# Kernel tuning notes

Hardware: AMD Instinct MI355X
Metric: run time of the kernel (lower is better)

## Reference

```python
import jax, jax.numpy as jnp
import numpy as np

B, N, F, G, M, E = 8, 512, 64, 64, 4, 4
L0 = 256          # NodeEmbedding hidden width (layers[0])
ALPHA = 0.5
EPS = 1e-5        # BatchNorm eps (training mode, batch stats)
NEG = -9e15       # masked-out logit value from the torch code


def _glorot(key, shape):
    # matches repo's glorot(): U(-s, s), s = sqrt(6/(fan_in+fan_out)) on last two dims
    s = float(np.sqrt(6.0 / (shape[-2] + shape[-1])))
    return jax.random.uniform(key, shape, minval=-s, maxval=s, dtype=jnp.float32)


def _xavier(key, shape, gain=1.0):
    s = gain * float(np.sqrt(6.0 / (shape[-2] + shape[-1])))
    return jax.random.uniform(key, shape, minval=-s, maxval=s, dtype=jnp.float32)


def setup_inputs() -> dict:
    key = jax.random.key(0)
    ks = jax.random.split(key, 8)
    A = jax.random.randint(ks[0], (B, E, N, N), 0, 2).astype(jnp.int32)  # dense 0/1 adjacency per edge cat
    X = jax.random.normal(ks[1], (B, N, F), dtype=jnp.float32)
    Ws = _glorot(ks[2], (E, M * F, G))                     # per-edge-cat stacked multi-head proj
    a1 = _xavier(ks[3], (E, M * G, 1), gain=1.414)
    a2 = _xavier(ks[4], (E, M * G, 1), gain=1.414)
    W_emb1 = _xavier(ks[5], (F, M * E * G))                # Embedding1: Linear(M*E*G -> F, no bias)
    W2a = _xavier(ks[6], (L0, F))                          # NodeEmbedding linear0: F -> L0
    W2b = _xavier(ks[7], (F, L0))                          # NodeEmbedding linear1: L0 -> F
    return {"A": A, "X": X, "Ws": Ws, "a1": a1, "a2": a2,
            "W_emb1": W_emb1, "W2a": W2a, "W2b": W2b, "mini_batch": 1}


def _bn(x):
    # BatchNorm1d in training mode, weight=1, bias=0, biased variance
    mu = x.mean(axis=0)
    var = x.var(axis=0)
    return (x - mu) / jnp.sqrt(var + EPS)


def reference(A, X, Ws, a1, a2, W_emb1, W2a, W2b, mini_batch):
    Wsr = Ws.reshape(E, M, F, G)        # per edge-cat, per head projection
    a1r = a1.reshape(E, M, G)
    a2r = a2.reshape(E, M, G)

    # Wh[b,e,m,n,g] = X[b] @ Ws[e] head m
    Wh = jnp.einsum('bnf,emfg->bemng', X, Wsr)
    s1 = jnp.einsum('bemng,emg->bemn', Wh, a1r)
    s2 = jnp.einsum('bemng,emg->bemn', Wh, a2r)
    logits = jax.nn.leaky_relu(s1[..., :, None] + s2[..., None, :])  # [B,E,M,N,N]
    logits = jnp.where(A[:, :, None, :, :] > 0, logits, NEG)
    att = jax.nn.softmax(logits, axis=-1)                            # softmax over neighbors (dim=1 of NxN)
    H = jax.nn.elu(jnp.einsum('bemij,bemjg->bemig', att, Wh))        # [B,E,M,N,G]

    # layout matches torch reshapes: feature index = m*(E*G) + e*G + g
    H = H.transpose(0, 3, 2, 1, 4).reshape(B * N, M * E * G)
    H = H @ W_emb1.T                                                 # Embedding1
    Xf = X.reshape(B * N, F)
    H = _bn((1.0 - ALPHA) * H + ALPHA * Xf)                          # BN1 with residual mix

    # NodeEmbedding: Linear -> BN -> ELU -> Linear
    Z = jax.nn.elu(_bn(H @ W2a.T)) @ W2b.T
    Z = _bn(H + Z)                                                   # BN2 residual
    return Z.reshape(B, N, F)
```

## Files before the change

### kernel.cpp

```cpp
#include <hip/hip_runtime.h>
#include <math.h>

#define B_   8
#define N_   512
#define F_   64
#define G_   64
#define M_   4
#define E_   4
#define MEG  1024

typedef __attribute__((ext_vector_type(8))) __bf16 bf16x8;
typedef __attribute__((ext_vector_type(4))) float f32x4;
typedef unsigned short ush;

static __device__ __forceinline__ ush bfu(float x) { __bf16 h = (__bf16)x; return __builtin_bit_cast(ush, h); }
static __device__ __forceinline__ bf16x8 asbf(int4 v) { return __builtin_bit_cast(bf16x8, v); }
static __device__ __forceinline__ bf16x8 cvt8(float4 a, float4 b) {
  bf16x8 r;
  r[0] = (__bf16)a.x; r[1] = (__bf16)a.y; r[2] = (__bf16)a.z; r[3] = (__bf16)a.w;
  r[4] = (__bf16)b.x; r[5] = (__bf16)b.y; r[6] = (__bf16)b.z; r[7] = (__bf16)b.w;
  return r;
}

__global__ void __launch_bounds__(256) k1_wh(const float* __restrict__ X, const float* __restrict__ Ws,
                                             const float* __restrict__ a1, const float* __restrict__ a2,
                                             const int* __restrict__ A,
                                             ush* __restrict__ WhF, float* __restrict__ s1,
                                             float2* __restrict__ E2, unsigned* __restrict__ Amask) {
  const int tid = threadIdx.x, lane = tid & 63, w = tid >> 6, c = lane & 15, grp = lane >> 4;
  const int blk = blockIdx.x, nt = blk & 7, em = (blk >> 3) & 15, b = blk >> 7;
  const int n0 = nt * 64, bem = b * 16 + em;

  __shared__ __align__(16) ush xl[2][4][64][8];
  __shared__ __align__(16) ush wl[2][4][64][8];
  __shared__ float c1b[64], c2b[64];
  __shared__ __align__(16) ush st[4096];

  {
    const int w2 = blk * 256 + tid;
    const int* ap = A + (w2 >> 4) * 512 + (w2 & 15) * 32;
    unsigned bits = 0;
#pragma unroll
    for (int kq = 0; kq < 32; kq += 4) {
      int4 v = *(const int4*)(ap + kq);
      bits |= (v.x > 0 ? 1u : 0u) << kq;
      bits |= (v.y > 0 ? 1u : 0u) << (kq + 1);
      bits |= (v.z > 0 ? 1u : 0u) << (kq + 2);
      bits |= (v.w > 0 ? 1u : 0u) << (kq + 3);
    }
    Amask[w2] = bits;
  }

  {
    const int row = tid >> 2, cg = tid & 3;
    const int t = row >> 4, cc = row & 15;
    const float* xp = X + (b * 512 + n0 + row) * 64 + cg * 16;
#pragma unroll
    for (int q4 = 0; q4 < 4; ++q4) {
      float4 v = ((const float4*)xp)[q4];
      float vals[4] = {v.x, v.y, v.z, v.w};
#pragma unroll
      for (int u = 0; u < 4; ++u) {
        const int f = cg * 16 + q4 * 4 + u;
        xl[f >> 5][t][((f >> 3) & 3) * 16 + cc][f & 7] = bfu(vals[u]);
      }
    }
  }
  {
    const int f = tid >> 2, gq = tid & 3;
    const int kk = f >> 5, gg = (f >> 3) & 3, ii = f & 7;
    const float* wp = Ws + em * 4096 + f * 64 + gq * 16;
    const float* p1 = a1 + em * 64 + gq * 16;
    const float* p2 = a2 + em * 64 + gq * 16;
    float d1 = 0.f, d2 = 0.f;
#pragma unroll
    for (int q4 = 0; q4 < 4; ++q4) {
      float4 v  = ((const float4*)wp)[q4];
      float4 va = ((const float4*)p1)[q4];
      float4 vb = ((const float4*)p2)[q4];
      float vals[4] = {v.x, v.y, v.z, v.w};
      float aa[4] = {va.x, va.y, va.z, va.w};
      float bb[4] = {vb.x, vb.y, vb.z, vb.w};
#pragma unroll
      for (int u = 0; u < 4; ++u) {
        const int g = gq * 16 + q4 * 4 + u;
        wl[kk][g >> 4][gg * 16 + (g & 15)][ii] = bfu(vals[u]);
        d1 = fmaf(vals[u], aa[u], d1);
        d2 = fmaf(vals[u], bb[u], d2);
      }
    }
    d1 += __shfl_xor(d1, 1); d1 += __shfl_xor(d1, 2);
    d2 += __shfl_xor(d2, 1); d2 += __shfl_xor(d2, 2);
    if (gq == 0) { c1b[f] = d1; c2b[f] = d2; }
  }
  __syncthreads();

  f32x4 acc[4] = {};
#pragma unroll
  for (int kk = 0; kk < 2; ++kk) {
    bf16x8 af = asbf(*(const int4*)&wl[kk][w][lane][0]);
#pragma unroll
    for (int t = 0; t < 4; ++t) {
      bf16x8 bv = asbf(*(const int4*)&xl[kk][t][lane][0]);
      acc[t] = __builtin_amdgcn_mfma_f32_16x16x32_bf16(af, bv, acc[t], 0, 0, 0);
    }
  }
#pragma unroll
  for (int t = 0; t < 4; ++t) {
    const int sl = t >> 1;
    const int gp = (t & 1) * 2 + (c >> 3);
    const int ii = c & 7;
#pragma unroll
    for (int r = 0; r < 4; ++r)
      st[sl * 2048 + w * 512 + (gp * 16 + grp * 4 + r) * 8 + ii] = bfu(acc[t][r]);
  }
  if (w == 0) {
    f32x4 sacc[4] = {};
#pragma unroll
    for (int kk = 0; kk < 2; ++kk) {
      bf16x8 af;
#pragma unroll
      for (int i = 0; i < 8; ++i) {
        const int f = kk * 32 + grp * 8 + i;
        float v = (c == 0) ? c1b[f] : (c == 1) ? c2b[f] : 0.f;
        af[i] = (__bf16)v;
      }
#pragma unroll
      for (int t = 0; t < 4; ++t) {
        bf16x8 bv = asbf(*(const int4*)&xl[kk][t][lane][0]);
        sacc[t] = __builtin_amdgcn_mfma_f32_16x16x32_bf16(af, bv, sacc[t], 0, 0, 0);
      }
    }
    if (grp == 0) {
#pragma unroll
      for (int t = 0; t < 4; ++t) {
        float s2v = sacc[t][1];
        s1[bem * 512 + n0 + t * 16 + c] = sacc[t][0];
        E2[bem * 512 + n0 + t * 16 + c] = make_float2(__expf(s2v), __expf(0.01f * s2v));
      }
    }
  }
  __syncthreads();
  {
    int4* dst = (int4*)(WhF + bem * 32768 + nt * 4096);
    const int4* src = (const int4*)st;
    dst[tid * 2]     = src[tid * 2];
    dst[tid * 2 + 1] = src[tid * 2 + 1];
  }
}

__global__ void __launch_bounds__(256) k2_attn(const unsigned* __restrict__ Amask,
                                               const ush* __restrict__ WhF,
                                               const float* __restrict__ s1,
                                               const float2* __restrict__ E2,
                                               ush* __restrict__ Hb) {
  const int tid = threadIdx.x, lane = tid & 63, m = tid >> 6;
  const int grp = lane >> 4, col = lane & 15;
  const int blk = blockIdx.x;
  const int xcd = blk & 7, kk2 = blk >> 3;
  const int be = xcd * 4 + (kk2 >> 5), itile = kk2 & 31;
  const int b = be >> 2, e = be & 3;
  const int i0 = itile * 16;
  const int bem = be * 4 + m;

  __shared__ unsigned maskw[16][17];
  __shared__ float2 e2l[4][512];

  {
    const int row = tid >> 4, cc = tid & 15;
    maskw[row][cc] = Amask[(be * 512 + i0 + row) * 16 + cc];
  }
  {
    const float2* e2g = E2 + bem * 512;
#pragma unroll
    for (int t = 0; t < 8; ++t) e2l[m][t * 64 + lane] = e2g[t * 64 + lane];
  }
  __syncthreads();

  const float s1row = s1[bem * N_ + i0 + col];
  const float e1p = __expf(s1row);
  const float e1n = __expf(0.01f * s1row);
  const float te  = __expf(-s1row);

  const ush* whb = WhF + bem * 32768 + lane * 8;
  f32x4 acc0 = {0.f, 0.f, 0.f, 0.f};
  f32x4 acc1 = acc0, acc2 = acc0, acc3 = acc0, accs = acc0;
  bf16x8 ones;
#pragma unroll
  for (int i = 0; i < 8; ++i) ones[i] = (__bf16)1.0f;

  int4 c0 = *(const int4*)(whb + 0);
  int4 c1 = *(const int4*)(whb + 512);
  int4 c2 = *(const int4*)(whb + 1024);
  int4 c3 = *(const int4*)(whb + 1536);
#pragma unroll 4
  for (int s = 0; s < 16; ++s) {
    const int noff = ((s + 1) & 15) * 2048;
    int4 n0 = *(const int4*)(whb + noff);
    int4 n1 = *(const int4*)(whb + noff + 512);
    int4 n2 = *(const int4*)(whb + noff + 1024);
    int4 n3 = *(const int4*)(whb + noff + 1536);

    unsigned mb = maskw[col][s] >> (grp * 8);
    const float2* ep = &e2l[m][s * 32 + grp * 8];
    bf16x8 af;
#pragma unroll
    for (int i = 0; i < 8; ++i) {
      float2 q = ep[i];
      float p = (q.x > te) ? q.x * e1p : q.y * e1n;
      p = ((mb >> i) & 1u) ? p : 0.f;
      af[i] = (__bf16)p;
    }
    accs = __builtin_amdgcn_mfma_f32_16x16x32_bf16(af, ones, accs, 0, 0, 0);
    acc0 = __builtin_amdgcn_mfma_f32_16x16x32_bf16(af, asbf(c0), acc0, 0, 0, 0);
    acc1 = __builtin_amdgcn_mfma_f32_16x16x32_bf16(af, asbf(c1), acc1, 0, 0, 0);
    acc2 = __builtin_amdgcn_mfma_f32_16x16x32_bf16(af, asbf(c2), acc2, 0, 0, 0);
    acc3 = __builtin_amdgcn_mfma_f32_16x16x32_bf16(af, asbf(c3), acc3, 0, 0, 0);
    c0 = n0; c1 = n1; c2 = n2; c3 = n3;
  }

  ush* op = Hb + (b * N_ + i0 + grp * 4) * MEG + m * 256 + e * 64 + col;
#pragma unroll
  for (int r = 0; r < 4; ++r) {
    float sv2 = accs[r];
    float inv = sv2 > 0.f ? 1.f / sv2 : 0.f;
    float v0 = acc0[r] * inv; v0 = v0 > 0.f ? v0 : expm1f(v0);
    float v1 = acc1[r] * inv; v1 = v1 > 0.f ? v1 : expm1f(v1);
    float v2 = acc2[r] * inv; v2 = v2 > 0.f ? v2 : expm1f(v2);
    float v3 = acc3[r] * inv; v3 = v3 > 0.f ? v3 : expm1f(v3);
    op[r * MEG + 0]  = bfu(v0);
    op[r * MEG + 16] = bfu(v1);
    op[r * MEG + 32] = bfu(v2);
    op[r * MEG + 48] = bfu(v3);
  }
}

__global__ void __launch_bounds__(256) k3_emb(const ush* __restrict__ Hb, const float* __restrict__ W_emb1,
                                              const float* __restrict__ X, float* __restrict__ R,
                                              float* __restrict__ P2R) {
  const int tid = threadIdx.x, lane = tid & 63, w = tid >> 6, c = lane & 15, grp = lane >> 4;
  const int r0 = blockIdx.x * 16;
  const ush* ha = Hb + (r0 + c) * 1024 + grp * 8;
  const float* wbf = W_emb1 + (w * 16 + c) * 1024 + grp * 8;
  f32x4 accA = {}, accB = {};
#pragma unroll 8
  for (int kk = 0; kk < 32; kk += 2) {
    bf16x8 w0 = cvt8(*(const float4*)(wbf + kk * 32),      *(const float4*)(wbf + kk * 32 + 4));
    bf16x8 w1 = cvt8(*(const float4*)(wbf + kk * 32 + 32), *(const float4*)(wbf + kk * 32 + 36));
    accA = __builtin_amdgcn_mfma_f32_16x16x32_bf16(asbf(*(const int4*)(ha + kk * 32)), w0, accA, 0, 0, 0);
    accB = __builtin_amdgcn_mfma_f32_16x16x32_bf16(asbf(*(const int4*)(ha + kk * 32 + 32)), w1, accB, 0, 0, 0);
  }
  f32x4 acc = accA + accB;
  const int col = w * 16 + c;
  float s = 0.f, q = 0.f;
#pragma unroll
  for (int r = 0; r < 4; ++r) {
    int row = r0 + grp * 4 + r;
    float v = 0.5f * acc[r] + 0.5f * X[row * 64 + col];
    R[row * 64 + col] = v;
    s += v; q = fmaf(v, v, q);
  }
  s += __shfl_xor(s, 16); s += __shfl_xor(s, 32);
  q += __shfl_xor(q, 16); q += __shfl_xor(q, 32);
  if (grp == 0) { P2R[blockIdx.x * 128 + col] = s; P2R[blockIdx.x * 128 + 64 + col] = q; }
}

__global__ void __launch_bounds__(256) k4_node1(const float* __restrict__ R, const float* __restrict__ P2R,
                                                const float* __restrict__ W2a,
                                                float* __restrict__ T, float* __restrict__ P2T) {
  const int tid = threadIdx.x, lane = tid & 63, w = tid >> 6, c = lane & 15, grp = lane >> 4;
  const int r0 = blockIdx.x * 16, cb = w * 64;
  __shared__ float muR[64], rsR[64];
  if (tid < 128) {
    const int cc = tid & 63;
    float a = 0.f;
    for (int bk = 0; bk < 256; ++bk) a += P2R[bk * 128 + tid];
    if (tid < 64) muR[cc] = a * (1.f / 4096.f); else rsR[cc] = a;
  }
  __syncthreads();
  if (tid < 64) {
    float m = muR[tid];
    float v = rsR[tid] * (1.f / 4096.f) - m * m;
    rsR[tid] = rsqrtf(v + 1e-5f);
  }
  __syncthreads();

  f32x4 acc[4] = {};
#pragma unroll
  for (int kk = 0; kk < 2; ++kk) {
    const float* rp = R + (r0 + c) * 64 + kk * 32 + grp * 8;
    float4 v0 = *(const float4*)rp;
    float4 v1 = *(const float4*)(rp + 4);
    float vv[8] = {v0.x, v0.y, v0.z, v0.w, v1.x, v1.y, v1.z, v1.w};
    bf16x8 af;
#pragma unroll
    for (int i = 0; i < 8; ++i) {
      int f = kk * 32 + grp * 8 + i;
      af[i] = (__bf16)((vv[i] - muR[f]) * rsR[f]);
    }
#pragma unroll
    for (int ct = 0; ct < 4; ++ct) {
      const float* wp = W2a + (cb + ct * 16 + c) * 64 + kk * 32 + grp * 8;
      bf16x8 bv = cvt8(*(const float4*)wp, *(const float4*)(wp + 4));
      acc[ct] = __builtin_amdgcn_mfma_f32_16x16x32_bf16(af, bv, acc[ct], 0, 0, 0);
    }
  }
#pragma unroll
  for (int ct = 0; ct < 4; ++ct) {
    const int col = cb + ct * 16 + c;
    float s = 0.f, q = 0.f;
#pragma unroll
    for (int r = 0; r < 4; ++r) {
      float v = acc[ct][r];
      T[(r0 + grp * 4 + r) * 256 + col] = v;
      s += v; q = fmaf(v, v, q);
    }
    s += __shfl_xor(s, 16); s += __shfl_xor(s, 32);
    q += __shfl_xor(q, 16); q += __shfl_xor(q, 32);
    if (grp == 0) { P2T[blockIdx.x * 512 + col] = s; P2T[blockIdx.x * 512 + 256 + col] = q; }
  }
}

__global__ void __launch_bounds__(256) k5_node2(const float* __restrict__ T, const float* __restrict__ P2T,
                                                const float* __restrict__ W2b,
                                                const float* __restrict__ R, const float* __restrict__ P2R,
                                                float* __restrict__ S, float* __restrict__ P2S) {
  const int tid = threadIdx.x, lane = tid & 63, w = tid >> 6, c = lane & 15, grp = lane >> 4;
  const int r0 = blockIdx.x * 16;
  __shared__ float muT[256], rsT[256], muR[64], rsR[64];
  {
    float s = 0.f, q = 0.f;
    for (int bk = 0; bk < 256; ++bk) {
      s += P2T[bk * 512 + tid];
      q += P2T[bk * 512 + 256 + tid];
    }
    float m = s * (1.f / 4096.f);
    float v = q * (1.f / 4096.f) - m * m;
    muT[tid] = m; rsT[tid] = rsqrtf(v + 1e-5f);
  }
  if (tid < 128) {
    const int cc = tid & 63;
    float a = 0.f;
    for (int bk = 0; bk < 256; ++bk) a += P2R[bk * 128 + tid];
    if (tid < 64) muR[cc] = a * (1.f / 4096.f); else rsR[cc] = a;
  }
  __syncthreads();
  if (tid < 64) {
    float m = muR[tid];
    float v = rsR[tid] * (1.f / 4096.f) - m * m;
    rsR[tid] = rsqrtf(v + 1e-5f);
  }
  __syncthreads();

  f32x4 accA = {}, accB = {};
  const float* wrow = W2b + (w * 16 + c) * 256 + grp * 8;
  const float* trow = T + (r0 + c) * 256 + grp * 8;
#pragma unroll
  for (int kk = 0; kk < 8; ++kk) {
    float4 v0 = *(const float4*)(trow + kk * 32);
    float4 v1 = *(const float4*)(trow + kk * 32 + 4);
    float vv[8] = {v0.x, v0.y, v0.z, v0.w, v1.x, v1.y, v1.z, v1.w};
    bf16x8 af;
#pragma unroll
    for (int i = 0; i < 8; ++i) {
      int u = kk * 32 + grp * 8 + i;
      float t = (vv[i] - muT[u]) * rsT[u];
      t = t > 0.f ? t : expm1f(t);
      af[i] = (__bf16)t;
    }
    bf16x8 bv = cvt8(*(const float4*)(wrow + kk * 32), *(const float4*)(wrow + kk * 32 + 4));
    if (kk & 1) accB = __builtin_amdgcn_mfma_f32_16x16x32_bf16(af, bv, accB, 0, 0, 0);
    else        accA = __builtin_amdgcn_mfma_f32_16x16x32_bf16(af, bv, accA, 0, 0, 0);
  }
  f32x4 acc = accA + accB;
  const int col = w * 16 + c;
  const float mu = muR[col], rsv = rsR[col];
  float s = 0.f, q = 0.f;
#pragma unroll
  for (int r = 0; r < 4; ++r) {
    int row = r0 + grp * 4 + r;
    float v = acc[r] + (R[row * 64 + col] - mu) * rsv;
    S[row * 64 + col] = v;
    s += v; q = fmaf(v, v, q);
  }
  s += __shfl_xor(s, 16); s += __shfl_xor(s, 32);
  q += __shfl_xor(q, 16); q += __shfl_xor(q, 32);
  if (grp == 0) { P2S[blockIdx.x * 128 + col] = s; P2S[blockIdx.x * 128 + 64 + col] = q; }
}

__global__ void __launch_bounds__(256) k6_bn(const float* __restrict__ S, const float* __restrict__ P2S,
                                             float* __restrict__ out) {
  const int tid = threadIdx.x;
  const int r0 = blockIdx.x * 16;
  __shared__ float muS[64], rsS[64];
  if (tid < 128) {
    const int cc = tid & 63;
    float a = 0.f;
    for (int bk = 0; bk < 256; ++bk) a += P2S[bk * 128 + tid];
    if (tid < 64) muS[cc] = a * (1.f / 4096.f); else rsS[cc] = a;
  }
  __syncthreads();
  if (tid < 64) {
    float m = muS[tid];
    float v = rsS[tid] * (1.f / 4096.f) - m * m;
    rsS[tid] = rsqrtf(v + 1e-5f);
  }
  __syncthreads();
  const int f0 = (tid * 4) & 63;
  float4 v = *(const float4*)(S + r0 * 64 + tid * 4);
  float4 o;
  o.x = (v.x - muS[f0 + 0]) * rsS[f0 + 0];
  o.y = (v.y - muS[f0 + 1]) * rsS[f0 + 1];
  o.z = (v.z - muS[f0 + 2]) * rsS[f0 + 2];
  o.w = (v.w - muS[f0 + 3]) * rsS[f0 + 3];
  *(float4*)(out + r0 * 64 + tid * 4) = o;
}

extern "C" void kernel_launch(void* const* d_in, const int* in_sizes, int n_in,
                              void* d_out, int out_size, void* d_ws, size_t ws_size,
                              hipStream_t stream) {
  const int*   A      = (const int*)d_in[0];
  const float* X      = (const float*)d_in[1];
  const float* Ws     = (const float*)d_in[2];
  const float* a1     = (const float*)d_in[3];
  const float* a2     = (const float*)d_in[4];
  const float* W_emb1 = (const float*)d_in[5];
  const float* W2a    = (const float*)d_in[6];
  const float* W2b    = (const float*)d_in[7];
  float* out = (float*)d_out;

  float* ws = (float*)d_ws;
  ush*   Hb    = (ush*)d_ws;
  ush*   WhF   = (ush*)(ws + 2097152);
  float* s1    = ws + 4194304;
  float2* E2   = (float2*)(ws + 4259840);
  float* R     = ws + 4612096;
  float* T     = ws + 4874240;
  float* S     = ws + 5922816;
  float* P2R   = ws + 6184960;
  float* P2T   = ws + 6217728;
  float* P2S   = ws + 6348800;
  unsigned* Amask = (unsigned*)R;

  k1_wh<<<1024, 256, 0, stream>>>(X, Ws, a1, a2, A, WhF, s1, E2, Amask);
  k2_attn<<<1024, 256, 0, stream>>>(Amask, WhF, s1, E2, Hb);
  k3_emb<<<256, 256, 0, stream>>>(Hb, W_emb1, X, R, P2R);
  k4_node1<<<256, 256, 0, stream>>>(R, P2R, W2a, T, P2T);
  k5_node2<<<256, 256, 0, stream>>>(T, P2T, W2b, R, P2R, S, P2S);
  k6_bn<<<256, 256, 0, stream>>>(S, P2S, out);
}
```

Baseline: 96.71 us.

## Process two 16-row tiles per attention block to reuse Wh loads

Each k2_attn block now computes 32 query rows as two 16-row MFMA tiles that share the same Wh B-operand fragments. The prefetch distance grows to two steps and the grid is halved to 512 blocks. This halves the global Wh traffic per output row and amortises the mask and E2 staging. In exchange it needs twice the accumulator registers, may lower occupancy, and leaves fewer blocks to spread across CUs.

```diff
diff --git a/kernel.cpp b/kernel.cpp
--- a/kernel.cpp
+++ b/kernel.cpp
@@ -158,17 +158,18 @@
   const int grp = lane >> 4, col = lane & 15;
   const int blk = blockIdx.x;
   const int xcd = blk & 7, kk2 = blk >> 3;
-  const int be = xcd * 4 + (kk2 >> 5), itile = kk2 & 31;
+  const int be = xcd * 4 + (kk2 >> 4), itile = kk2 & 15;
   const int b = be >> 2, e = be & 3;
-  const int i0 = itile * 16;
+  const int i0 = itile * 32;
   const int bem = be * 4 + m;
 
-  __shared__ unsigned maskw[16][17];
+  __shared__ unsigned maskw[32][17];
   __shared__ float2 e2l[4][512];
 
   {
-    const int row = tid >> 4, cc = tid & 15;
-    maskw[row][cc] = Amask[(be * 512 + i0 + row) * 16 + cc];
+    const int i_0 = tid, i_1 = tid + 256;
+    maskw[i_0 >> 4][i_0 & 15] = Amask[(be * 512 + i0 + (i_0 >> 4)) * 16 + (i_0 & 15)];
+    maskw[i_1 >> 4][i_1 & 15] = Amask[(be * 512 + i0 + (i_1 >> 4)) * 16 + (i_1 & 15)];
   }
   {
     const float2* e2g = E2 + bem * 512;
@@ -177,61 +178,94 @@
   }
   __syncthreads();
 
-  const float s1row = s1[bem * N_ + i0 + col];
-  const float e1p = __expf(s1row);
-  const float e1n = __expf(0.01f * s1row);
-  const float te  = __expf(-s1row);
+  const float s1A = s1[bem * N_ + i0 + col];
+  const float s1B = s1[bem * N_ + i0 + 16 + col];
+  const float e1pA = __expf(s1A), e1nA = __expf(0.01f * s1A), teA = __expf(-s1A);
+  const float e1pB = __expf(s1B), e1nB = __expf(0.01f * s1B), teB = __expf(-s1B);
 
   const ush* whb = WhF + bem * 32768 + lane * 8;
-  f32x4 acc0 = {0.f, 0.f, 0.f, 0.f};
-  f32x4 acc1 = acc0, acc2 = acc0, acc3 = acc0, accs = acc0;
+  f32x4 a0A = {0.f, 0.f, 0.f, 0.f};
+  f32x4 a1A = a0A, a2A = a0A, a3A = a0A, sA = a0A;
+  f32x4 a0B = a0A, a1B = a0A, a2B = a0A, a3B = a0A, sB = a0A;
   bf16x8 ones;
 #pragma unroll
   for (int i = 0; i < 8; ++i) ones[i] = (__bf16)1.0f;
 
-  int4 c0 = *(const int4*)(whb + 0);
-  int4 c1 = *(const int4*)(whb + 512);
-  int4 c2 = *(const int4*)(whb + 1024);
-  int4 c3 = *(const int4*)(whb + 1536);
-#pragma unroll 4
+  int4 cA0 = *(const int4*)(whb + 0);
+  int4 cA1 = *(const int4*)(whb + 512);
+  int4 cA2 = *(const int4*)(whb + 1024);
+  int4 cA3 = *(const int4*)(whb + 1536);
+  int4 cB0 = *(const int4*)(whb + 2048);
+  int4 cB1 = *(const int4*)(whb + 2560);
+  int4 cB2 = *(const int4*)(whb + 3072);
+  int4 cB3 = *(const int4*)(whb + 3584);
+#pragma unroll
   for (int s = 0; s < 16; ++s) {
-    const int noff = ((s + 1) & 15) * 2048;
+    const int noff = ((s + 2) & 15) * 2048;
     int4 n0 = *(const int4*)(whb + noff);
     int4 n1 = *(const int4*)(whb + noff + 512);
     int4 n2 = *(const int4*)(whb + noff + 1024);
     int4 n3 = *(const int4*)(whb + noff + 1536);
 
-    unsigned mb = maskw[col][s] >> (grp * 8);
+    const unsigned mbA = maskw[col][s] >> (grp * 8);
+    const unsigned mbB = maskw[col + 16][s] >> (grp * 8);
     const float2* ep = &e2l[m][s * 32 + grp * 8];
-    bf16x8 af;
+    bf16x8 afA, afB;
 #pragma unroll
     for (int i = 0; i < 8; ++i) {
       float2 q = ep[i];
-      float p = (q.x > te) ? q.x * e1p : q.y * e1n;
-      p = ((mb >> i) & 1u) ? p : 0.f;
-      af[i] = (__bf16)p;
-    }
-    accs = __builtin_amdgcn_mfma_f32_16x16x32_bf16(af, ones, accs, 0, 0, 0);
-    acc0 = __builtin_amdgcn_mfma_f32_16x16x32_bf16(af, asbf(c0), acc0, 0, 0, 0);
-    acc1 = __builtin_amdgcn_mfma_f32_16x16x32_bf16(af, asbf(c1), acc1, 0, 0, 0);
-    acc2 = __builtin_amdgcn_mfma_f32_16x16x32_bf16(af, asbf(c2), acc2, 0, 0, 0);
-    acc3 = __builtin_amdgcn_mfma_f32_16x16x32_bf16(af, asbf(c3), acc3, 0, 0, 0);
-    c0 = n0; c1 = n1; c2 = n2; c3 = n3;
-  }
-
-  ush* op = Hb + (b * N_ + i0 + grp * 4) * MEG + m * 256 + e * 64 + col;
-#pragma unroll
-  for (int r = 0; r < 4; ++r) {
-    float sv2 = accs[r];
-    float inv = sv2 > 0.f ? 1.f / sv2 : 0.f;
-    float v0 = acc0[r] * inv; v0 = v0 > 0.f ? v0 : expm1f(v0);
-    float v1 = acc1[r] * inv; v1 = v1 > 0.f ? v1 : expm1f(v1);
-    float v2 = acc2[r] * inv; v2 = v2 > 0.f ? v2 : expm1f(v2);
-    float v3 = acc3[r] * inv; v3 = v3 > 0.f ? v3 : expm1f(v3);
-    op[r * MEG + 0]  = bfu(v0);
-    op[r * MEG + 16] = bfu(v1);
-    op[r * MEG + 32] = bfu(v2);
-    op[r * MEG + 48] = bfu(v3);
+      float pA = (q.x > teA) ? q.x * e1pA : q.y * e1nA;
+      pA = ((mbA >> i) & 1u) ? pA : 0.f;
+      afA[i] = (__bf16)pA;
+      float pB = (q.x > teB) ? q.x * e1pB : q.y * e1nB;
+      pB = ((mbB >> i) & 1u) ? pB : 0.f;
+      afB[i] = (__bf16)pB;
+    }
+    sA  = __builtin_amdgcn_mfma_f32_16x16x32_bf16(afA, ones, sA, 0, 0, 0);
+    sB  = __builtin_amdgcn_mfma_f32_16x16x32_bf16(afB, ones, sB, 0, 0, 0);
+    a0A = __builtin_amdgcn_mfma_f32_16x16x32_bf16(afA, asbf(cA0), a0A, 0, 0, 0);
+    a0B = __builtin_amdgcn_mfma_f32_16x16x32_bf16(afB, asbf(cA0), a0B, 0, 0, 0);
+    a1A = __builtin_amdgcn_mfma_f32_16x16x32_bf16(afA, asbf(cA1), a1A, 0, 0, 0);
+    a1B = __builtin_amdgcn_mfma_f32_16x16x32_bf16(afB, asbf(cA1), a1B, 0, 0, 0);
+    a2A = __builtin_amdgcn_mfma_f32_16x16x32_bf16(afA, asbf(cA2), a2A, 0, 0, 0);
+    a2B = __builtin_amdgcn_mfma_f32_16x16x32_bf16(afB, asbf(cA2), a2B, 0, 0, 0);
+    a3A = __builtin_amdgcn_mfma_f32_16x16x32_bf16(afA, asbf(cA3), a3A, 0, 0, 0);
+    a3B = __builtin_amdgcn_mfma_f32_16x16x32_bf16(afB, asbf(cA3), a3B, 0, 0, 0);
+    cA0 = cB0; cA1 = cB1; cA2 = cB2; cA3 = cB3;
+    cB0 = n0;  cB1 = n1;  cB2 = n2;  cB3 = n3;
+  }
+
+  {
+    ush* op = Hb + (b * N_ + i0 + grp * 4) * MEG + m * 256 + e * 64 + col;
+#pragma unroll
+    for (int r = 0; r < 4; ++r) {
+      float sv = sA[r];
+      float inv = sv > 0.f ? 1.f / sv : 0.f;
+      float v0 = a0A[r] * inv; v0 = v0 > 0.f ? v0 : expm1f(v0);
+      float v1 = a1A[r] * inv; v1 = v1 > 0.f ? v1 : expm1f(v1);
+      float v2 = a2A[r] * inv; v2 = v2 > 0.f ? v2 : expm1f(v2);
+      float v3 = a3A[r] * inv; v3 = v3 > 0.f ? v3 : expm1f(v3);
+      op[r * MEG + 0]  = bfu(v0);
+      op[r * MEG + 16] = bfu(v1);
+      op[r * MEG + 32] = bfu(v2);
+      op[r * MEG + 48] = bfu(v3);
+    }
+  }
+  {
+    ush* op = Hb + (b * N_ + i0 + 16 + grp * 4) * MEG + m * 256 + e * 64 + col;
+#pragma unroll
+    for (int r = 0; r < 4; ++r) {
+      float sv = sB[r];
+      float inv = sv > 0.f ? 1.f / sv : 0.f;
+      float v0 = a0B[r] * inv; v0 = v0 > 0.f ? v0 : expm1f(v0);
+      float v1 = a1B[r] * inv; v1 = v1 > 0.f ? v1 : expm1f(v1);
+      float v2 = a2B[r] * inv; v2 = v2 > 0.f ? v2 : expm1f(v2);
+      float v3 = a3B[r] * inv; v3 = v3 > 0.f ? v3 : expm1f(v3);
+      op[r * MEG + 0]  = bfu(v0);
+      op[r * MEG + 16] = bfu(v1);
+      op[r * MEG + 32] = bfu(v2);
+      op[r * MEG + 48] = bfu(v3);
+    }
   }
 }
 
@@ -443,7 +477,7 @@
   unsigned* Amask = (unsigned*)R;
 
   k1_wh<<<1024, 256, 0, stream>>>(X, Ws, a1, a2, A, WhF, s1, E2, Amask);
-  k2_attn<<<1024, 256, 0, stream>>>(Amask, WhF, s1, E2, Hb);
+  k2_attn<<<512, 256, 0, stream>>>(Amask, WhF, s1, E2, Hb);
   k3_emb<<<256, 256, 0, stream>>>(Hb, W_emb1, X, R, P2R);
   k4_node1<<<256, 256, 0, stream>>>(R, P2R, W2a, T, P2T);
   k5_node2<<<256, 256, 0, stream>>>(T, P2T, W2b, R, P2R, S, P2S);
```

Result: no change. 96.92 us (+0.2%).

## Widen tail kernels to 512 threads with split-K and parallel BN stat reductions

Applied to the files above, without the earlier changes.

Doubles the block size of the embedding and node-MLP kernels. The matmuls are split along K across two wave groups and the partial sums are combined through shared memory. The per-block reduction of batch-norm partial statistics is spread over all threads in chunks instead of a serial 256-iteration loop by a few threads. This targets latency in these small tail kernels, which run only 256 blocks, at the cost of extra syncthreads and shared memory.

```diff
diff --git a/kernel.cpp b/kernel.cpp
--- a/kernel.cpp
+++ b/kernel.cpp
@@ -235,57 +235,84 @@
   }
 }
 
-__global__ void __launch_bounds__(256) k3_emb(const ush* __restrict__ Hb, const float* __restrict__ W_emb1,
+__global__ void __launch_bounds__(512) k3_emb(const ush* __restrict__ Hb, const float* __restrict__ W_emb1,
                                               const float* __restrict__ X, float* __restrict__ R,
                                               float* __restrict__ P2R) {
-  const int tid = threadIdx.x, lane = tid & 63, w = tid >> 6, c = lane & 15, grp = lane >> 4;
+  const int tid = threadIdx.x, lane = tid & 63, w8 = tid >> 6, c = lane & 15, grp = lane >> 4;
+  const int wcol = w8 & 3, khalf = w8 >> 2;
   const int r0 = blockIdx.x * 16;
-  const ush* ha = Hb + (r0 + c) * 1024 + grp * 8;
-  const float* wbf = W_emb1 + (w * 16 + c) * 1024 + grp * 8;
+  __shared__ float part[4][64][4];
+
+  const ush* ha = Hb + (r0 + c) * 1024 + khalf * 512 + grp * 8;
+  const float* wbf = W_emb1 + (wcol * 16 + c) * 1024 + khalf * 512 + grp * 8;
   f32x4 accA = {}, accB = {};
 #pragma unroll 8
-  for (int kk = 0; kk < 32; kk += 2) {
+  for (int kk = 0; kk < 16; kk += 2) {
     bf16x8 w0 = cvt8(*(const float4*)(wbf + kk * 32),      *(const float4*)(wbf + kk * 32 + 4));
     bf16x8 w1 = cvt8(*(const float4*)(wbf + kk * 32 + 32), *(const float4*)(wbf + kk * 32 + 36));
     accA = __builtin_amdgcn_mfma_f32_16x16x32_bf16(asbf(*(const int4*)(ha + kk * 32)), w0, accA, 0, 0, 0);
     accB = __builtin_amdgcn_mfma_f32_16x16x32_bf16(asbf(*(const int4*)(ha + kk * 32 + 32)), w1, accB, 0, 0, 0);
   }
   f32x4 acc = accA + accB;
-  const int col = w * 16 + c;
-  float s = 0.f, q = 0.f;
-#pragma unroll
-  for (int r = 0; r < 4; ++r) {
-    int row = r0 + grp * 4 + r;
-    float v = 0.5f * acc[r] + 0.5f * X[row * 64 + col];
-    R[row * 64 + col] = v;
-    s += v; q = fmaf(v, v, q);
-  }
-  s += __shfl_xor(s, 16); s += __shfl_xor(s, 32);
-  q += __shfl_xor(q, 16); q += __shfl_xor(q, 32);
-  if (grp == 0) { P2R[blockIdx.x * 128 + col] = s; P2R[blockIdx.x * 128 + 64 + col] = q; }
-}
-
-__global__ void __launch_bounds__(256) k4_node1(const float* __restrict__ R, const float* __restrict__ P2R,
+  if (khalf == 1) {
+#pragma unroll
+    for (int r = 0; r < 4; ++r) part[wcol][lane][r] = acc[r];
+  }
+  __syncthreads();
+  if (khalf == 0) {
+    const int col = wcol * 16 + c;
+    float s = 0.f, q = 0.f;
+#pragma unroll
+    for (int r = 0; r < 4; ++r) {
+      int row = r0 + grp * 4 + r;
+      float v = 0.5f * (acc[r] + part[wcol][lane][r]) + 0.5f * X[row * 64 + col];
+      R[row * 64 + col] = v;
+      s += v; q = fmaf(v, v, q);
+    }
+    s += __shfl_xor(s, 16); s += __shfl_xor(s, 32);
+    q += __shfl_xor(q, 16); q += __shfl_xor(q, 32);
+    if (grp == 0) { P2R[blockIdx.x * 128 + col] = s; P2R[blockIdx.x * 128 + 64 + col] = q; }
+  }
+}
+
+__global__ void __launch_bounds__(512) k4_node1(const float* __restrict__ R, const float* __restrict__ P2R,
                                                 const float* __restrict__ W2a,
                                                 float* __restrict__ T, float* __restrict__ P2T) {
-  const int tid = threadIdx.x, lane = tid & 63, w = tid >> 6, c = lane & 15, grp = lane >> 4;
-  const int r0 = blockIdx.x * 16, cb = w * 64;
+  const int tid = threadIdx.x, lane = tid & 63, w8 = tid >> 6, c = lane & 15, grp = lane >> 4;
+  const int r0 = blockIdx.x * 16, cb = w8 * 32;
   __shared__ float muR[64], rsR[64];
-  if (tid < 128) {
-    const int cc = tid & 63;
-    float a = 0.f;
-    for (int bk = 0; bk < 256; ++bk) a += P2R[bk * 128 + tid];
-    if (tid < 64) muR[cc] = a * (1.f / 4096.f); else rsR[cc] = a;
+  __shared__ float red8[8][64];
+  {
+    const int cc = tid & 63, ch = tid >> 6;
+    float a = 0.f;
+    for (int bk = ch * 32; bk < ch * 32 + 32; ++bk) a += P2R[bk * 128 + cc];
+    red8[ch][cc] = a;
   }
   __syncthreads();
   if (tid < 64) {
+    float a = 0.f;
+#pragma unroll
+    for (int ch = 0; ch < 8; ++ch) a += red8[ch][tid];
+    muR[tid] = a * (1.f / 4096.f);
+  }
+  __syncthreads();
+  {
+    const int cc = tid & 63, ch = tid >> 6;
+    float a = 0.f;
+    for (int bk = ch * 32; bk < ch * 32 + 32; ++bk) a += P2R[bk * 128 + 64 + cc];
+    red8[ch][cc] = a;
+  }
+  __syncthreads();
+  if (tid < 64) {
+    float a = 0.f;
+#pragma unroll
+    for (int ch = 0; ch < 8; ++ch) a += red8[ch][tid];
     float m = muR[tid];
-    float v = rsR[tid] * (1.f / 4096.f) - m * m;
-    rsR[tid] = rsqrtf(v + 1e-5f);
-  }
-  __syncthreads();
-
-  f32x4 acc[4] = {};
+    rsR[tid] = rsqrtf(a * (1.f / 4096.f) - m * m + 1e-5f);
+  }
+  __syncthreads();
+
+  f32x4 acc[2] = {};
 #pragma unroll
   for (int kk = 0; kk < 2; ++kk) {
     const float* rp = R + (r0 + c) * 64 + kk * 32 + grp * 8;
@@ -299,14 +326,14 @@
       af[i] = (__bf16)((vv[i] - muR[f]) * rsR[f]);
     }
 #pragma unroll
-    for (int ct = 0; ct < 4; ++ct) {
+    for (int ct = 0; ct < 2; ++ct) {
       const float* wp = W2a + (cb + ct * 16 + c) * 64 + kk * 32 + grp * 8;
       bf16x8 bv = cvt8(*(const float4*)wp, *(const float4*)(wp + 4));
       acc[ct] = __builtin_amdgcn_mfma_f32_16x16x32_bf16(af, bv, acc[ct], 0, 0, 0);
     }
   }
 #pragma unroll
-  for (int ct = 0; ct < 4; ++ct) {
+  for (int ct = 0; ct < 2; ++ct) {
     const int col = cb + ct * 16 + c;
     float s = 0.f, q = 0.f;
 #pragma unroll
@@ -321,42 +348,72 @@
   }
 }
 
-__global__ void __launch_bounds__(256) k5_node2(const float* __restrict__ T, const float* __restrict__ P2T,
+__global__ void __launch_bounds__(512) k5_node2(const float* __restrict__ T, const float* __restrict__ P2T,
                                                 const float* __restrict__ W2b,
                                                 const float* __restrict__ R, const float* __restrict__ P2R,
                                                 float* __restrict__ S, float* __restrict__ P2S) {
-  const int tid = threadIdx.x, lane = tid & 63, w = tid >> 6, c = lane & 15, grp = lane >> 4;
+  const int tid = threadIdx.x, lane = tid & 63, w8 = tid >> 6, c = lane & 15, grp = lane >> 4;
+  const int wcol = w8 & 3, khalf = w8 >> 2;
   const int r0 = blockIdx.x * 16;
   __shared__ float muT[256], rsT[256], muR[64], rsR[64];
-  {
-    float s = 0.f, q = 0.f;
-    for (int bk = 0; bk < 256; ++bk) {
-      s += P2T[bk * 512 + tid];
-      q += P2T[bk * 512 + 256 + tid];
-    }
-    float m = s * (1.f / 4096.f);
-    float v = q * (1.f / 4096.f) - m * m;
-    muT[tid] = m; rsT[tid] = rsqrtf(v + 1e-5f);
-  }
-  if (tid < 128) {
-    const int cc = tid & 63;
-    float a = 0.f;
-    for (int bk = 0; bk < 256; ++bk) a += P2R[bk * 128 + tid];
-    if (tid < 64) muR[cc] = a * (1.f / 4096.f); else rsR[cc] = a;
+  __shared__ float redT[2][256];
+  __shared__ float red8[8][64];
+  __shared__ float part[4][64][4];
+  {
+    const int cc = tid & 255, ch = tid >> 8;
+    float s = 0.f;
+    for (int bk = ch * 128; bk < ch * 128 + 128; ++bk) s += P2T[bk * 512 + cc];
+    redT[ch][cc] = s;
+  }
+  __syncthreads();
+  if (tid < 256) muT[tid] = (redT[0][tid] + redT[1][tid]) * (1.f / 4096.f);
+  __syncthreads();
+  {
+    const int cc = tid & 255, ch = tid >> 8;
+    float q = 0.f;
+    for (int bk = ch * 128; bk < ch * 128 + 128; ++bk) q += P2T[bk * 512 + 256 + cc];
+    redT[ch][cc] = q;
+  }
+  {
+    const int cc = tid & 63, ch = tid >> 6;
+    float s = 0.f;
+    for (int bk = ch * 32; bk < ch * 32 + 32; ++bk) s += P2R[bk * 128 + cc];
+    red8[ch][cc] = s;
+  }
+  __syncthreads();
+  if (tid < 256) {
+    float m = muT[tid];
+    rsT[tid] = rsqrtf((redT[0][tid] + redT[1][tid]) * (1.f / 4096.f) - m * m + 1e-5f);
+  }
+  if (tid >= 256 && tid < 320) {
+    const int cc = tid - 256;
+    float a = 0.f;
+#pragma unroll
+    for (int ch = 0; ch < 8; ++ch) a += red8[ch][cc];
+    muR[cc] = a * (1.f / 4096.f);
+  }
+  __syncthreads();
+  {
+    const int cc = tid & 63, ch = tid >> 6;
+    float q = 0.f;
+    for (int bk = ch * 32; bk < ch * 32 + 32; ++bk) q += P2R[bk * 128 + 64 + cc];
+    red8[ch][cc] = q;
   }
   __syncthreads();
   if (tid < 64) {
+    float a = 0.f;
+#pragma unroll
+    for (int ch = 0; ch < 8; ++ch) a += red8[ch][tid];
     float m = muR[tid];
-    float v = rsR[tid] * (1.f / 4096.f) - m * m;
-    rsR[tid] = rsqrtf(v + 1e-5f);
+    rsR[tid] = rsqrtf(a * (1.f / 4096.f) - m * m + 1e-5f);
   }
   __syncthreads();
 
   f32x4 accA = {}, accB = {};
-  const float* wrow = W2b + (w * 16 + c) * 256 + grp * 8;
+  const float* wrow = W2b + (wcol * 16 + c) * 256 + grp * 8;
   const float* trow = T + (r0 + c) * 256 + grp * 8;
 #pragma unroll
-  for (int kk = 0; kk < 8; ++kk) {
+  for (int kk = khalf * 4; kk < khalf * 4 + 4; ++kk) {
     float4 v0 = *(const float4*)(trow + kk * 32);
     float4 v1 = *(const float4*)(trow + kk * 32 + 4);
     float vv[8] = {v0.x, v0.y, v0.z, v0.w, v1.x, v1.y, v1.z, v1.w};
@@ -373,19 +430,26 @@
     else        accA = __builtin_amdgcn_mfma_f32_16x16x32_bf16(af, bv, accA, 0, 0, 0);
   }
   f32x4 acc = accA + accB;
-  const int col = w * 16 + c;
-  const float mu = muR[col], rsv = rsR[col];
-  float s = 0.f, q = 0.f;
-#pragma unroll
-  for (int r = 0; r < 4; ++r) {
-    int row = r0 + grp * 4 + r;
-    float v = acc[r] + (R[row * 64 + col] - mu) * rsv;
-    S[row * 64 + col] = v;
-    s += v; q = fmaf(v, v, q);
-  }
-  s += __shfl_xor(s, 16); s += __shfl_xor(s, 32);
-  q += __shfl_xor(q, 16); q += __shfl_xor(q, 32);
-  if (grp == 0) { P2S[blockIdx.x * 128 + col] = s; P2S[blockIdx.x * 128 + 64 + col] = q; }
+  if (khalf == 1) {
+#pragma unroll
+    for (int r = 0; r < 4; ++r) part[wcol][lane][r] = acc[r];
+  }
+  __syncthreads();
+  if (khalf == 0) {
+    const int col = wcol * 16 + c;
+    const float mu = muR[col], rsv = rsR[col];
+    float s = 0.f, q = 0.f;
+#pragma unroll
+    for (int r = 0; r < 4; ++r) {
+      int row = r0 + grp * 4 + r;
+      float v = acc[r] + part[wcol][lane][r] + (R[row * 64 + col] - mu) * rsv;
+      S[row * 64 + col] = v;
+      s += v; q = fmaf(v, v, q);
+    }
+    s += __shfl_xor(s, 16); s += __shfl_xor(s, 32);
+    q += __shfl_xor(q, 16); q += __shfl_xor(q, 32);
+    if (grp == 0) { P2S[blockIdx.x * 128 + col] = s; P2S[blockIdx.x * 128 + 64 + col] = q; }
+  }
 }
 
 __global__ void __launch_bounds__(256) k6_bn(const float* __restrict__ S, const float* __restrict__ P2S,
@@ -393,17 +457,27 @@
   const int tid = threadIdx.x;
   const int r0 = blockIdx.x * 16;
   __shared__ float muS[64], rsS[64];
-  if (tid < 128) {
-    const int cc = tid & 63;
-    float a = 0.f;
-    for (int bk = 0; bk < 256; ++bk) a += P2S[bk * 128 + tid];
-    if (tid < 64) muS[cc] = a * (1.f / 4096.f); else rsS[cc] = a;
+  __shared__ float red4[4][64];
+  {
+    const int cc = tid & 63, ch = tid >> 6;
+    float a = 0.f;
+    for (int bk = ch * 64; bk < ch * 64 + 64; ++bk) a += P2S[bk * 128 + cc];
+    red4[ch][cc] = a;
+  }
+  __syncthreads();
+  if (tid < 64) muS[tid] = (red4[0][tid] + red4[1][tid] + red4[2][tid] + red4[3][tid]) * (1.f / 4096.f);
+  __syncthreads();
+  {
+    const int cc = tid & 63, ch = tid >> 6;
+    float a = 0.f;
+    for (int bk = ch * 64; bk < ch * 64 + 64; ++bk) a += P2S[bk * 128 + 64 + cc];
+    red4[ch][cc] = a;
   }
   __syncthreads();
   if (tid < 64) {
+    float q = red4[0][tid] + red4[1][tid] + red4[2][tid] + red4[3][tid];
     float m = muS[tid];
-    float v = rsS[tid] * (1.f / 4096.f) - m * m;
-    rsS[tid] = rsqrtf(v + 1e-5f);
+    rsS[tid] = rsqrtf(q * (1.f / 4096.f) - m * m + 1e-5f);
   }
   __syncthreads();
   const int f0 = (tid * 4) & 63;
@@ -444,8 +518,8 @@
 
   k1_wh<<<1024, 256, 0, stream>>>(X, Ws, a1, a2, A, WhF, s1, E2, Amask);
   k2_attn<<<1024, 256, 0, stream>>>(Amask, WhF, s1, E2, Hb);
-  k3_emb<<<256, 256, 0, stream>>>(Hb, W_emb1, X, R, P2R);
-  k4_node1<<<256, 256, 0, stream>>>(R, P2R, W2a, T, P2T);
-  k5_node2<<<256, 256, 0, stream>>>(T, P2T, W2b, R, P2R, S, P2S);
+  k3_emb<<<256, 512, 0, stream>>>(Hb, W_emb1, X, R, P2R);
+  k4_node1<<<256, 512, 0, stream>>>(R, P2R, W2a, T, P2T);
+  k5_node2<<<256, 512, 0, stream>>>(T, P2T, W2b, R, P2R, S, P2S);
   k6_bn<<<256, 256, 0, stream>>>(S, P2S, out);
 }
```

Result: faster. 83.20 us (median of 2 runs) (-14.0%).
